# Kernel tuning notes

Measured on AMD Instinct MI355X. Metric: run time of the kernel, lower is better.

The kernel has to match this reference:

```python
import jax, jax.numpy as jnp
import numpy as np


def setup_inputs() -> dict:
    key = jax.random.key(0)
    ks = jax.random.split(key, 5)
    B, H, W, C, R = 4, 64, 64, 256, 32
    x = jax.random.normal(ks[0], (B, H, W, C), dtype=jnp.float32)
    # 1x1 conv kernels stored as [C_in, C_out] matrices (equivalent math)
    w_f = jax.random.normal(ks[1], (C, R), dtype=jnp.float32) * (1.0 / np.sqrt(C))
    w_g = jax.random.normal(ks[2], (C, R), dtype=jnp.float32) * (1.0 / np.sqrt(C))
    w_h = jax.random.normal(ks[3], (C, R), dtype=jnp.float32) * (1.0 / np.sqrt(C))
    w_v = jax.random.normal(ks[4], (R, C), dtype=jnp.float32) * (1.0 / np.sqrt(R))
    gamma = jnp.zeros((1,), dtype=jnp.float32)
    return {"x": x, "w_f": w_f, "w_g": w_g, "w_h": w_h, "w_v": w_v, "gamma": gamma}


def reference(x, w_f, w_g, w_h, w_v, gamma):
    B, H, W, C = x.shape
    N = H * W
    xt = x.reshape(B, N, C)                       # flatten spatial tokens
    f = jnp.einsum('bnc,cr->bnr', xt, w_f)        # 1x1 conv == token-wise matmul
    g = jnp.einsum('bnc,cr->bnr', xt, w_g)
    h = jnp.einsum('bnc,cr->bnr', xt, w_h)
    scores = jnp.einsum('bnr,bmr->bnm', f, g)     # [B, N, N]
    # NOTE: original softmaxes over axis=1 (the query/row axis), not axis=-1
    attn = jax.nn.softmax(scores, axis=1)
    y = jnp.einsum('bnm,bmr->bnr', attn, h)       # [B, N, R]
    y = jnp.einsum('bnr,rc->bnc', y, w_v)         # output 1x1 conv
    y = y.reshape(B, H, W, C)
    return gamma * y + x
```

## Files before the change

kernel.cpp:

```cpp
#include <hip/hip_runtime.h>


#define BB 4
#define NN 4096
#define CC 256
#define RR 32
#define CSEG 4
#define LOG2E 1.44269504088896340736f

typedef short short8 __attribute__((ext_vector_type(8)));
typedef short short4v __attribute__((ext_vector_type(4)));
typedef unsigned short ushort8 __attribute__((ext_vector_type(8)));
typedef float floatx4 __attribute__((ext_vector_type(4)));

#define MFMA16 __builtin_amdgcn_mfma_f32_16x16x32_bf16
#define MFMA16K __builtin_amdgcn_mfma_f32_16x16x16bf16_1k

static __device__ __forceinline__ unsigned short f2bf(float f) {
  union { float f; unsigned u; } v; v.f = f;
  const unsigned r = v.u + 0x7fffu + ((v.u >> 16) & 1u);
  return (unsigned short)(r >> 16);
}
static __device__ __forceinline__ unsigned bfpack(float lo, float hi) {
  return __builtin_amdgcn_perm(__float_as_uint(hi), __float_as_uint(lo), 0x07060302u);
}

__global__ __launch_bounds__(256) void k_prep(
    const float* __restrict__ wf, const float* __restrict__ wg,
    const float* __restrict__ wh, const float* __restrict__ wv,
    unsigned short* __restrict__ wfrag, unsigned short* __restrict__ wvfrag) {
  const int idx = blockIdx.x * 256 + threadIdx.x;
  const int lane = (idx >> 3) & 63;
  const int j = idx & 7;
  const int col = lane & 15, q = lane >> 4;
  if (idx < 24576) {
    const int mat = idx >> 13;
    const int fid = (idx >> 9) & 15;
    const int kc = fid >> 1, nt = fid & 1;
    const float* w = (mat == 0) ? wf : ((mat == 1) ? wg : wh);
    wfrag[idx] = f2bf(w[(kc * 32 + q * 8 + j) * RR + nt * 16 + col]);
  } else {
    const int r = idx - 24576;
    const int t = (r >> 9) & 15;
    wvfrag[r] = f2bf(wv[(q * 8 + j) * CC + t * 16 + col]);
  }
}

__global__ __launch_bounds__(256) void k_fgh(
    const float* __restrict__ x, const unsigned short* __restrict__ wfrag,
    unsigned short* __restrict__ f16, unsigned short* __restrict__ g16,
    unsigned short* __restrict__ hT16) {
  __shared__ unsigned short wflds[24576];
  const int tid = threadIdx.x, lane = tid & 63, wave = tid >> 6;
  const int col = lane & 15, q = lane >> 4;
  {
    const uint4* src = (const uint4*)wfrag;
    uint4* dst = (uint4*)wflds;
#pragma unroll
    for (int i = 0; i < 12; ++i) dst[tid + i * 256] = src[tid + i * 256];
  }
  __syncthreads();
  const int t0 = blockIdx.x * 64 + wave * 16;
  short8 af[8];
  const float* xr = x + (long)(t0 + col) * CC + q * 8;
#pragma unroll
  for (int kc = 0; kc < 8; ++kc) {
    float tmp[8];
    *(float4*)(tmp) = *(const float4*)(xr + kc * 32);
    *(float4*)(tmp + 4) = *(const float4*)(xr + kc * 32 + 4);
    short8 o;
#pragma unroll
    for (int j = 0; j < 8; ++j) o[j] = (short)f2bf(tmp[j]);
    af[kc] = o;
  }
  const floatx4 zero = {0.f, 0.f, 0.f, 0.f};
  floatx4 acc[3][2];
#pragma unroll
  for (int m = 0; m < 3; ++m) { acc[m][0] = zero; acc[m][1] = zero; }
#pragma unroll
  for (int kc = 0; kc < 8; ++kc) {
#pragma unroll
    for (int mat = 0; mat < 3; ++mat) {
#pragma unroll
      for (int nt = 0; nt < 2; ++nt) {
        const short8 bf = *(const short8*)(wflds + (mat * 16 + kc * 2 + nt) * 512 + lane * 8);
        acc[mat][nt] = MFMA16(af[kc], bf, acc[mat][nt], 0, 0, 0);
      }
    }
  }
  const int b = t0 >> 12;
#pragma unroll
  for (int nt = 0; nt < 2; ++nt) {
#pragma unroll
    for (int r = 0; r < 4; ++r) {
      const int tok = t0 + q * 4 + r;
      const int n = nt * 16 + col;
      f16[(long)tok * RR + n] = f2bf(acc[0][nt][r] * LOG2E);
      g16[(long)tok * RR + n] = f2bf(acc[1][nt][r]);
      const int tl = tok & (NN - 1);
      const int sp = (tl & ~31) | (q << 3) | ((tl & 16) >> 2) | r;
      hT16[((long)b * RR + n) * NN + sp] = f2bf(acc[2][nt][r]);
    }
  }
}

__global__ __launch_bounds__(256) void k_colsum(
    const unsigned short* __restrict__ f16, const unsigned short* __restrict__ g16,
    float* __restrict__ psum) {
  const int tid = threadIdx.x, lane = tid & 63, wave = tid >> 6;
  const int col = lane & 15, q = lane >> 4;
  const int mblk = blockIdx.x & 31;
  const int b = (blockIdx.x >> 5) & 3;
  const int seg = blockIdx.x >> 7;
  const int m0 = mblk * 128 + wave * 32;
  const short8 bg1 = *(const short8*)(g16 + ((long)(b * NN + m0 + col)) * RR + q * 8);
  const short8 bg2 = *(const short8*)(g16 + ((long)(b * NN + m0 + 16 + col)) * RR + q * 8);
  const floatx4 zero = {0.f, 0.f, 0.f, 0.f};
  float s1 = 0.f, s2 = 0.f;
  const unsigned short* fb = f16 + ((long)b * NN + seg * (NN / CSEG)) * RR;
#pragma unroll 4
  for (int n = 0; n < NN / CSEG; n += 16) {
    const short8 af = *(const short8*)(fb + (long)(n + col) * RR + q * 8);
    const floatx4 d1 = MFMA16(af, bg1, zero, 0, 0, 0);
    const floatx4 d2 = MFMA16(af, bg2, zero, 0, 0, 0);
    s1 += __builtin_amdgcn_exp2f(d1[0]) + __builtin_amdgcn_exp2f(d1[1]) +
          __builtin_amdgcn_exp2f(d1[2]) + __builtin_amdgcn_exp2f(d1[3]);
    s2 += __builtin_amdgcn_exp2f(d2[0]) + __builtin_amdgcn_exp2f(d2[1]) +
          __builtin_amdgcn_exp2f(d2[2]) + __builtin_amdgcn_exp2f(d2[3]);
  }
  s1 += __shfl_xor(s1, 16); s1 += __shfl_xor(s1, 32);
  s2 += __shfl_xor(s2, 16); s2 += __shfl_xor(s2, 32);
  if (lane < 16) {
    psum[(long)seg * (BB * NN) + b * NN + m0 + lane] = s1;
    psum[(long)seg * (BB * NN) + b * NN + m0 + 16 + lane] = s2;
  }
}

__global__ __launch_bounds__(256) void k_scaleh(
    const float* __restrict__ psum, unsigned short* __restrict__ hT16) {
  const long i8 = ((long)blockIdx.x * 256 + threadIdx.x) * 8;
  const int b = (int)(i8 >> 17);
  const int m = (int)(i8 & (NN - 1));
  const int lo = (m & ~31) | ((m & 24) >> 1);
  float cs[8] = {0.f, 0.f, 0.f, 0.f, 0.f, 0.f, 0.f, 0.f};
#pragma unroll
  for (int sg = 0; sg < CSEG; ++sg) {
    const float* p = psum + (long)sg * (BB * NN) + b * NN;
    const float4 a = *(const float4*)(p + lo);
    const float4 c = *(const float4*)(p + lo + 16);
    cs[0] += a.x; cs[1] += a.y; cs[2] += a.z; cs[3] += a.w;
    cs[4] += c.x; cs[5] += c.y; cs[6] += c.z; cs[7] += c.w;
  }
  const ushort8 hv = *(const ushort8*)(hT16 + i8);
  ushort8 o;
#pragma unroll
  for (int j = 0; j < 8; ++j) {
    const float h = __uint_as_float(((unsigned)hv[j]) << 16);
    o[j] = f2bf(h * __builtin_amdgcn_rcpf(cs[j]));
  }
  *(ushort8*)(hT16 + i8) = o;
}

__global__ __launch_bounds__(512, 4) void k_pvout(
    const unsigned short* __restrict__ f16, const unsigned short* __restrict__ g16,
    const unsigned short* __restrict__ hT16, const unsigned short* __restrict__ wvfrag,
    const float* __restrict__ x, const float* __restrict__ gamma,
    float* __restrict__ out) {
  __shared__ float ylds[8][32 * 36];
  __shared__ float sc_all[8][16 * 36];
  const int tid = threadIdx.x, lane = tid & 63, wave = tid >> 6;
  const int col = lane & 15, q = lane >> 4;
  const int b = blockIdx.x >> 7;
  const int t0 = (blockIdx.x & 127) * 32;
  const floatx4 zero = {0.f, 0.f, 0.f, 0.f};
  const short8 af1 = *(const short8*)(f16 + ((long)(b * NN + t0 + col)) * RR + q * 8);
  const short8 af2 = *(const short8*)(f16 + ((long)(b * NN + t0 + 16 + col)) * RR + q * 8);
  floatx4 a11 = zero, a12 = zero, a21 = zero, a22 = zero;
  const unsigned short* gb = g16 + (long)b * NN * RR;
  const unsigned short* hb = hT16 + (long)b * RR * NN;
  const int mq = wave * 512;
#pragma unroll 2
  for (int mi = 0; mi < 512; mi += 32) {
    const int m0 = mq + mi;
    const short8 bg1 = *(const short8*)(gb + (long)(m0 + col) * RR + q * 8);
    const short8 bg2 = *(const short8*)(gb + (long)(m0 + 16 + col) * RR + q * 8);
    const short8 hv1 = *(const short8*)(hb + (long)col * NN + m0 + q * 8);
    const short8 hv2 = *(const short8*)(hb + (long)(col + 16) * NN + m0 + q * 8);
    const floatx4 d00 = MFMA16(bg1, af1, zero, 0, 0, 0);
    const floatx4 d01 = MFMA16(bg2, af1, zero, 0, 0, 0);
    const floatx4 d10 = MFMA16(bg1, af2, zero, 0, 0, 0);
    const floatx4 d11 = MFMA16(bg2, af2, zero, 0, 0, 0);
    union PU { unsigned u[2]; short4v s; } p00, p01, p10, p11;
    p00.u[0] = bfpack(__builtin_amdgcn_exp2f(d00[0]), __builtin_amdgcn_exp2f(d00[1]));
    p00.u[1] = bfpack(__builtin_amdgcn_exp2f(d00[2]), __builtin_amdgcn_exp2f(d00[3]));
    p01.u[0] = bfpack(__builtin_amdgcn_exp2f(d01[0]), __builtin_amdgcn_exp2f(d01[1]));
    p01.u[1] = bfpack(__builtin_amdgcn_exp2f(d01[2]), __builtin_amdgcn_exp2f(d01[3]));
    p10.u[0] = bfpack(__builtin_amdgcn_exp2f(d10[0]), __builtin_amdgcn_exp2f(d10[1]));
    p10.u[1] = bfpack(__builtin_amdgcn_exp2f(d10[2]), __builtin_amdgcn_exp2f(d10[3]));
    p11.u[0] = bfpack(__builtin_amdgcn_exp2f(d11[0]), __builtin_amdgcn_exp2f(d11[1]));
    p11.u[1] = bfpack(__builtin_amdgcn_exp2f(d11[2]), __builtin_amdgcn_exp2f(d11[3]));
    const short4v bh1lo = __builtin_shufflevector(hv1, hv1, 0, 1, 2, 3);
    const short4v bh1hi = __builtin_shufflevector(hv1, hv1, 4, 5, 6, 7);
    const short4v bh2lo = __builtin_shufflevector(hv2, hv2, 0, 1, 2, 3);
    const short4v bh2hi = __builtin_shufflevector(hv2, hv2, 4, 5, 6, 7);
    a11 = MFMA16K(p00.s, bh1lo, a11, 0, 0, 0);
    a11 = MFMA16K(p01.s, bh1hi, a11, 0, 0, 0);
    a12 = MFMA16K(p00.s, bh2lo, a12, 0, 0, 0);
    a12 = MFMA16K(p01.s, bh2hi, a12, 0, 0, 0);
    a21 = MFMA16K(p10.s, bh1lo, a21, 0, 0, 0);
    a21 = MFMA16K(p11.s, bh1hi, a21, 0, 0, 0);
    a22 = MFMA16K(p10.s, bh2lo, a22, 0, 0, 0);
    a22 = MFMA16K(p11.s, bh2hi, a22, 0, 0, 0);
  }
  {
    float* yp = &ylds[wave][0];
#pragma unroll
    for (int r = 0; r < 4; ++r) {
      yp[(q * 4 + r) * 36 + col] = a11[r];
      yp[(q * 4 + r) * 36 + col + 16] = a12[r];
      yp[(16 + q * 4 + r) * 36 + col] = a21[r];
      yp[(16 + q * 4 + r) * 36 + col + 16] = a22[r];
    }
  }
  __syncthreads();
  {
    const int tile = wave & 1, hh = wave >> 1;
    float s[8] = {0.f, 0.f, 0.f, 0.f, 0.f, 0.f, 0.f, 0.f};
#pragma unroll
    for (int w2 = 0; w2 < 8; ++w2) {
      const float* yp = &ylds[w2][(tile * 16 + col) * 36 + q * 8];
      const float4 u0 = *(const float4*)yp;
      const float4 u1 = *(const float4*)(yp + 4);
      s[0] += u0.x; s[1] += u0.y; s[2] += u0.z; s[3] += u0.w;
      s[4] += u1.x; s[5] += u1.y; s[6] += u1.z; s[7] += u1.w;
    }
    short8 ay;
#pragma unroll
    for (int j = 0; j < 8; ++j) ay[j] = (short)f2bf(s[j]);
    const float gm = gamma[0];
    float* sc = &sc_all[wave][0];
    const int row = lane >> 2, c4 = (lane & 3) * 4;
#pragma unroll
    for (int tp = 0; tp < 4; tp += 2) {
      const short8 bw0 = *(const short8*)(wvfrag + (hh * 4 + tp) * 512 + lane * 8);
      const short8 bw1 = *(const short8*)(wvfrag + (hh * 4 + tp + 1) * 512 + lane * 8);
      const floatx4 d0 = MFMA16(ay, bw0, zero, 0, 0, 0);
      const floatx4 d1 = MFMA16(ay, bw1, zero, 0, 0, 0);
#pragma unroll
      for (int r = 0; r < 4; ++r) {
        sc[(q * 4 + r) * 36 + col] = d0[r];
        sc[(q * 4 + r) * 36 + col + 16] = d1[r];
      }
#pragma unroll
      for (int j = 0; j < 2; ++j) {
        const float4 v = *(const float4*)(sc + row * 36 + c4 + j * 16);
        const long gidx = (long)(b * NN + t0 + tile * 16 + row) * CC +
                          hh * 64 + tp * 16 + j * 16 + c4;
        const float4 xv = *(const float4*)(x + gidx);
        float4 o;
        o.x = gm * v.x + xv.x; o.y = gm * v.y + xv.y;
        o.z = gm * v.z + xv.z; o.w = gm * v.w + xv.w;
        *(float4*)(out + gidx) = o;
      }
    }
  }
}

extern "C" void kernel_launch(void* const* d_in, const int* in_sizes, int n_in,
                              void* d_out, int out_size, void* d_ws, size_t ws_size,
                              hipStream_t stream) {
  const float* x = (const float*)d_in[0];
  const float* wf = (const float*)d_in[1];
  const float* wg = (const float*)d_in[2];
  const float* wh = (const float*)d_in[3];
  const float* wv = (const float*)d_in[4];
  const float* gamma = (const float*)d_in[5];
  float* out = (float*)d_out;

  unsigned short* f16 = (unsigned short*)d_ws;
  unsigned short* g16 = f16 + (long)BB * NN * RR;
  unsigned short* hT16 = g16 + (long)BB * NN * RR;
  unsigned short* wfrag = hT16 + (long)BB * NN * RR;
  unsigned short* wvfrag = wfrag + 24576;
  float* psum = (float*)(wvfrag + 8192);

  k_prep<<<128, 256, 0, stream>>>(wf, wg, wh, wv, wfrag, wvfrag);
  k_fgh<<<BB * NN / 64, 256, 0, stream>>>(x, wfrag, f16, g16, hT16);
  k_colsum<<<CSEG * BB * 32, 256, 0, stream>>>(f16, g16, psum);
  k_scaleh<<<BB * RR * NN / 2048, 256, 0, stream>>>(psum, hT16);
  k_pvout<<<BB * 128, 512, 0, stream>>>(f16, g16, hT16, wvfrag, x, gamma, out);
}
```

Before: 125.0 us.

## Fold softmax normalization into MFMA accumulator and drop prep and scale kernels

```diff
diff --git a/kernel.cpp b/kernel.cpp
--- a/kernel.cpp
+++ b/kernel.cpp
@@ -5,7 +5,6 @@
 #define NN 4096
 #define CC 256
 #define RR 32
-#define CSEG 4
 #define LOG2E 1.44269504088896340736f
 
 typedef short short8 __attribute__((ext_vector_type(8)));
@@ -25,41 +24,31 @@
   return __builtin_amdgcn_perm(__float_as_uint(hi), __float_as_uint(lo), 0x07060302u);
 }
 
-__global__ __launch_bounds__(256) void k_prep(
-    const float* __restrict__ wf, const float* __restrict__ wg,
-    const float* __restrict__ wh, const float* __restrict__ wv,
-    unsigned short* __restrict__ wfrag, unsigned short* __restrict__ wvfrag) {
-  const int idx = blockIdx.x * 256 + threadIdx.x;
-  const int lane = (idx >> 3) & 63;
-  const int j = idx & 7;
-  const int col = lane & 15, q = lane >> 4;
-  if (idx < 24576) {
-    const int mat = idx >> 13;
-    const int fid = (idx >> 9) & 15;
-    const int kc = fid >> 1, nt = fid & 1;
-    const float* w = (mat == 0) ? wf : ((mat == 1) ? wg : wh);
-    wfrag[idx] = f2bf(w[(kc * 32 + q * 8 + j) * RR + nt * 16 + col]);
-  } else {
-    const int r = idx - 24576;
-    const int t = (r >> 9) & 15;
-    wvfrag[r] = f2bf(wv[(q * 8 + j) * CC + t * 16 + col]);
-  }
-}
-
 __global__ __launch_bounds__(256) void k_fgh(
-    const float* __restrict__ x, const unsigned short* __restrict__ wfrag,
+    const float* __restrict__ x, const float* __restrict__ wf,
+    const float* __restrict__ wg, const float* __restrict__ wh,
     unsigned short* __restrict__ f16, unsigned short* __restrict__ g16,
     unsigned short* __restrict__ hT16) {
   __shared__ unsigned short wflds[24576];
   const int tid = threadIdx.x, lane = tid & 63, wave = tid >> 6;
   const int col = lane & 15, q = lane >> 4;
   {
-    const uint4* src = (const uint4*)wfrag;
-    uint4* dst = (uint4*)wflds;
-#pragma unroll
-    for (int i = 0; i < 12; ++i) dst[tid + i * 256] = src[tid + i * 256];
-  }
-  __syncthreads();
+    const float* mats[3] = {wf, wg, wh};
+#pragma unroll
+    for (int mat = 0; mat < 3; ++mat) {
+      const float* w = mats[mat];
+#pragma unroll 4
+      for (int i = 0; i < 32; ++i) {
+        const int idx = mat * 8192 + i * 256 + tid;
+        const int fid = (idx >> 9) & 15;
+        const int kc = fid >> 1, nt = fid & 1;
+        const int l2 = (idx >> 3) & 63;
+        const int c2 = l2 & 15, q2 = l2 >> 4;
+        const int j = idx & 7;
+        wflds[idx] = f2bf(w[(kc * 32 + q2 * 8 + j) * RR + nt * 16 + c2]);
+      }
+    }
+  }
   const int t0 = blockIdx.x * 64 + wave * 16;
   short8 af[8];
   const float* xr = x + (long)(t0 + col) * CC + q * 8;
@@ -73,6 +62,7 @@
     for (int j = 0; j < 8; ++j) o[j] = (short)f2bf(tmp[j]);
     af[kc] = o;
   }
+  __syncthreads();
   const floatx4 zero = {0.f, 0.f, 0.f, 0.f};
   floatx4 acc[3][2];
 #pragma unroll
@@ -106,20 +96,19 @@
 
 __global__ __launch_bounds__(256) void k_colsum(
     const unsigned short* __restrict__ f16, const unsigned short* __restrict__ g16,
-    float* __restrict__ psum) {
+    float* __restrict__ nlg2cs) {
+  __shared__ float red[4][32];
   const int tid = threadIdx.x, lane = tid & 63, wave = tid >> 6;
   const int col = lane & 15, q = lane >> 4;
-  const int mblk = blockIdx.x & 31;
-  const int b = (blockIdx.x >> 5) & 3;
-  const int seg = blockIdx.x >> 7;
-  const int m0 = mblk * 128 + wave * 32;
+  const int b = blockIdx.x >> 7;
+  const int m0 = (blockIdx.x & 127) * 32;
   const short8 bg1 = *(const short8*)(g16 + ((long)(b * NN + m0 + col)) * RR + q * 8);
   const short8 bg2 = *(const short8*)(g16 + ((long)(b * NN + m0 + 16 + col)) * RR + q * 8);
   const floatx4 zero = {0.f, 0.f, 0.f, 0.f};
   float s1 = 0.f, s2 = 0.f;
-  const unsigned short* fb = f16 + ((long)b * NN + seg * (NN / CSEG)) * RR;
+  const unsigned short* fb = f16 + ((long)b * NN + wave * (NN / 4)) * RR;
 #pragma unroll 4
-  for (int n = 0; n < NN / CSEG; n += 16) {
+  for (int n = 0; n < NN / 4; n += 16) {
     const short8 af = *(const short8*)(fb + (long)(n + col) * RR + q * 8);
     const floatx4 d1 = MFMA16(af, bg1, zero, 0, 0, 0);
     const floatx4 d2 = MFMA16(af, bg2, zero, 0, 0, 0);
@@ -131,53 +120,46 @@
   s1 += __shfl_xor(s1, 16); s1 += __shfl_xor(s1, 32);
   s2 += __shfl_xor(s2, 16); s2 += __shfl_xor(s2, 32);
   if (lane < 16) {
-    psum[(long)seg * (BB * NN) + b * NN + m0 + lane] = s1;
-    psum[(long)seg * (BB * NN) + b * NN + m0 + 16 + lane] = s2;
-  }
-}
-
-__global__ __launch_bounds__(256) void k_scaleh(
-    const float* __restrict__ psum, unsigned short* __restrict__ hT16) {
-  const long i8 = ((long)blockIdx.x * 256 + threadIdx.x) * 8;
-  const int b = (int)(i8 >> 17);
-  const int m = (int)(i8 & (NN - 1));
-  const int lo = (m & ~31) | ((m & 24) >> 1);
-  float cs[8] = {0.f, 0.f, 0.f, 0.f, 0.f, 0.f, 0.f, 0.f};
-#pragma unroll
-  for (int sg = 0; sg < CSEG; ++sg) {
-    const float* p = psum + (long)sg * (BB * NN) + b * NN;
-    const float4 a = *(const float4*)(p + lo);
-    const float4 c = *(const float4*)(p + lo + 16);
-    cs[0] += a.x; cs[1] += a.y; cs[2] += a.z; cs[3] += a.w;
-    cs[4] += c.x; cs[5] += c.y; cs[6] += c.z; cs[7] += c.w;
-  }
-  const ushort8 hv = *(const ushort8*)(hT16 + i8);
-  ushort8 o;
-#pragma unroll
-  for (int j = 0; j < 8; ++j) {
-    const float h = __uint_as_float(((unsigned)hv[j]) << 16);
-    o[j] = f2bf(h * __builtin_amdgcn_rcpf(cs[j]));
-  }
-  *(ushort8*)(hT16 + i8) = o;
+    red[wave][lane] = s1;
+    red[wave][lane + 16] = s2;
+  }
+  __syncthreads();
+  if (tid < 32) {
+    const float cs = red[0][tid] + red[1][tid] + red[2][tid] + red[3][tid];
+    nlg2cs[(long)b * NN + m0 + tid] = -__builtin_amdgcn_logf(cs);
+  }
 }
 
 __global__ __launch_bounds__(512, 4) void k_pvout(
     const unsigned short* __restrict__ f16, const unsigned short* __restrict__ g16,
-    const unsigned short* __restrict__ hT16, const unsigned short* __restrict__ wvfrag,
-    const float* __restrict__ x, const float* __restrict__ gamma,
-    float* __restrict__ out) {
+    const unsigned short* __restrict__ hT16, const float* __restrict__ nlg2cs,
+    const float* __restrict__ wv, const float* __restrict__ x,
+    const float* __restrict__ gamma, float* __restrict__ out) {
   __shared__ float ylds[8][32 * 36];
   __shared__ float sc_all[8][16 * 36];
+  __shared__ unsigned short wvlds[8192];
   const int tid = threadIdx.x, lane = tid & 63, wave = tid >> 6;
   const int col = lane & 15, q = lane >> 4;
   const int b = blockIdx.x >> 7;
   const int t0 = (blockIdx.x & 127) * 32;
   const floatx4 zero = {0.f, 0.f, 0.f, 0.f};
+  {
+#pragma unroll 4
+    for (int i = 0; i < 16; ++i) {
+      const int idx = i * 512 + tid;
+      const int t = idx >> 9;
+      const int l2 = (idx >> 3) & 63;
+      const int c2 = l2 & 15, q2 = l2 >> 4;
+      const int j = idx & 7;
+      wvlds[idx] = f2bf(wv[(q2 * 8 + j) * CC + t * 16 + c2]);
+    }
+  }
   const short8 af1 = *(const short8*)(f16 + ((long)(b * NN + t0 + col)) * RR + q * 8);
   const short8 af2 = *(const short8*)(f16 + ((long)(b * NN + t0 + 16 + col)) * RR + q * 8);
   floatx4 a11 = zero, a12 = zero, a21 = zero, a22 = zero;
   const unsigned short* gb = g16 + (long)b * NN * RR;
   const unsigned short* hb = hT16 + (long)b * RR * NN;
+  const float* csb = nlg2cs + (long)b * NN;
   const int mq = wave * 512;
 #pragma unroll 2
   for (int mi = 0; mi < 512; mi += 32) {
@@ -186,10 +168,12 @@
     const short8 bg2 = *(const short8*)(gb + (long)(m0 + 16 + col) * RR + q * 8);
     const short8 hv1 = *(const short8*)(hb + (long)col * NN + m0 + q * 8);
     const short8 hv2 = *(const short8*)(hb + (long)(col + 16) * NN + m0 + q * 8);
-    const floatx4 d00 = MFMA16(bg1, af1, zero, 0, 0, 0);
-    const floatx4 d01 = MFMA16(bg2, af1, zero, 0, 0, 0);
-    const floatx4 d10 = MFMA16(bg1, af2, zero, 0, 0, 0);
-    const floatx4 d11 = MFMA16(bg2, af2, zero, 0, 0, 0);
+    const floatx4 cm0 = *(const floatx4*)(csb + m0 + q * 4);
+    const floatx4 cm1 = *(const floatx4*)(csb + m0 + 16 + q * 4);
+    const floatx4 d00 = MFMA16(bg1, af1, cm0, 0, 0, 0);
+    const floatx4 d01 = MFMA16(bg2, af1, cm1, 0, 0, 0);
+    const floatx4 d10 = MFMA16(bg1, af2, cm0, 0, 0, 0);
+    const floatx4 d11 = MFMA16(bg2, af2, cm1, 0, 0, 0);
     union PU { unsigned u[2]; short4v s; } p00, p01, p10, p11;
     p00.u[0] = bfpack(__builtin_amdgcn_exp2f(d00[0]), __builtin_amdgcn_exp2f(d00[1]));
     p00.u[1] = bfpack(__builtin_amdgcn_exp2f(d00[2]), __builtin_amdgcn_exp2f(d00[3]));
@@ -242,8 +226,8 @@
     const int row = lane >> 2, c4 = (lane & 3) * 4;
 #pragma unroll
     for (int tp = 0; tp < 4; tp += 2) {
-      const short8 bw0 = *(const short8*)(wvfrag + (hh * 4 + tp) * 512 + lane * 8);
-      const short8 bw1 = *(const short8*)(wvfrag + (hh * 4 + tp + 1) * 512 + lane * 8);
+      const short8 bw0 = *(const short8*)(wvlds + (hh * 4 + tp) * 512 + lane * 8);
+      const short8 bw1 = *(const short8*)(wvlds + (hh * 4 + tp + 1) * 512 + lane * 8);
       const floatx4 d0 = MFMA16(ay, bw0, zero, 0, 0, 0);
       const floatx4 d1 = MFMA16(ay, bw1, zero, 0, 0, 0);
 #pragma unroll
@@ -280,13 +264,9 @@
   unsigned short* f16 = (unsigned short*)d_ws;
   unsigned short* g16 = f16 + (long)BB * NN * RR;
   unsigned short* hT16 = g16 + (long)BB * NN * RR;
-  unsigned short* wfrag = hT16 + (long)BB * NN * RR;
-  unsigned short* wvfrag = wfrag + 24576;
-  float* psum = (float*)(wvfrag + 8192);
-
-  k_prep<<<128, 256, 0, stream>>>(wf, wg, wh, wv, wfrag, wvfrag);
-  k_fgh<<<BB * NN / 64, 256, 0, stream>>>(x, wfrag, f16, g16, hT16);
-  k_colsum<<<CSEG * BB * 32, 256, 0, stream>>>(f16, g16, psum);
-  k_scaleh<<<BB * RR * NN / 2048, 256, 0, stream>>>(psum, hT16);
-  k_pvout<<<BB * 128, 512, 0, stream>>>(f16, g16, hT16, wvfrag, x, gamma, out);
-}
+  float* nlg2cs = (float*)(hT16 + (long)BB * NN * RR);
+
+  k_fgh<<<BB * NN / 64, 256, 0, stream>>>(x, wf, wg, wh, f16, g16, hT16);
+  k_colsum<<<BB * NN / 32, 256, 0, stream>>>(f16, g16, nlg2cs);
+  k_pvout<<<BB * 128, 512, 0, stream>>>(f16, g16, hT16, nlg2cs, wv, x, gamma, out);
+}
```

Measured after the change: 132.1 us. +5.7%, slower.

## Fold column-sum normalization into attention as log bias, drop scale-h kernel

Applied to the files above, without the earlier changes.

```diff
diff --git a/kernel.cpp b/kernel.cpp
--- a/kernel.cpp
+++ b/kernel.cpp
@@ -107,19 +107,21 @@
 __global__ __launch_bounds__(256) void k_colsum(
     const unsigned short* __restrict__ f16, const unsigned short* __restrict__ g16,
     float* __restrict__ psum) {
+  __shared__ float red[4][32];
   const int tid = threadIdx.x, lane = tid & 63, wave = tid >> 6;
   const int col = lane & 15, q = lane >> 4;
-  const int mblk = blockIdx.x & 31;
-  const int b = (blockIdx.x >> 5) & 3;
-  const int seg = blockIdx.x >> 7;
-  const int m0 = mblk * 128 + wave * 32;
+  const int mblk = blockIdx.x & 127;
+  const int b = (blockIdx.x >> 7) & 3;
+  const int seg = blockIdx.x >> 9;
+  const int m0 = mblk * 32;
   const short8 bg1 = *(const short8*)(g16 + ((long)(b * NN + m0 + col)) * RR + q * 8);
   const short8 bg2 = *(const short8*)(g16 + ((long)(b * NN + m0 + 16 + col)) * RR + q * 8);
   const floatx4 zero = {0.f, 0.f, 0.f, 0.f};
   float s1 = 0.f, s2 = 0.f;
-  const unsigned short* fb = f16 + ((long)b * NN + seg * (NN / CSEG)) * RR;
+  const unsigned short* fb =
+      f16 + ((long)b * NN + seg * (NN / CSEG) + wave * (NN / CSEG / 4)) * RR;
 #pragma unroll 4
-  for (int n = 0; n < NN / CSEG; n += 16) {
+  for (int n = 0; n < NN / CSEG / 4; n += 16) {
     const short8 af = *(const short8*)(fb + (long)(n + col) * RR + q * 8);
     const floatx4 d1 = MFMA16(af, bg1, zero, 0, 0, 0);
     const floatx4 d2 = MFMA16(af, bg2, zero, 0, 0, 0);
@@ -131,54 +133,49 @@
   s1 += __shfl_xor(s1, 16); s1 += __shfl_xor(s1, 32);
   s2 += __shfl_xor(s2, 16); s2 += __shfl_xor(s2, 32);
   if (lane < 16) {
-    psum[(long)seg * (BB * NN) + b * NN + m0 + lane] = s1;
-    psum[(long)seg * (BB * NN) + b * NN + m0 + 16 + lane] = s2;
-  }
-}
-
-__global__ __launch_bounds__(256) void k_scaleh(
-    const float* __restrict__ psum, unsigned short* __restrict__ hT16) {
-  const long i8 = ((long)blockIdx.x * 256 + threadIdx.x) * 8;
-  const int b = (int)(i8 >> 17);
-  const int m = (int)(i8 & (NN - 1));
-  const int lo = (m & ~31) | ((m & 24) >> 1);
-  float cs[8] = {0.f, 0.f, 0.f, 0.f, 0.f, 0.f, 0.f, 0.f};
-#pragma unroll
-  for (int sg = 0; sg < CSEG; ++sg) {
-    const float* p = psum + (long)sg * (BB * NN) + b * NN;
-    const float4 a = *(const float4*)(p + lo);
-    const float4 c = *(const float4*)(p + lo + 16);
-    cs[0] += a.x; cs[1] += a.y; cs[2] += a.z; cs[3] += a.w;
-    cs[4] += c.x; cs[5] += c.y; cs[6] += c.z; cs[7] += c.w;
-  }
-  const ushort8 hv = *(const ushort8*)(hT16 + i8);
-  ushort8 o;
-#pragma unroll
-  for (int j = 0; j < 8; ++j) {
-    const float h = __uint_as_float(((unsigned)hv[j]) << 16);
-    o[j] = f2bf(h * __builtin_amdgcn_rcpf(cs[j]));
-  }
-  *(ushort8*)(hT16 + i8) = o;
+    red[wave][lane] = s1;
+    red[wave][lane + 16] = s2;
+  }
+  __syncthreads();
+  if (tid < 32) {
+    psum[(long)seg * (BB * NN) + b * NN + m0 + tid] =
+        red[0][tid] + red[1][tid] + red[2][tid] + red[3][tid];
+  }
 }
 
 __global__ __launch_bounds__(512, 4) void k_pvout(
     const unsigned short* __restrict__ f16, const unsigned short* __restrict__ g16,
-    const unsigned short* __restrict__ hT16, const unsigned short* __restrict__ wvfrag,
-    const float* __restrict__ x, const float* __restrict__ gamma,
-    float* __restrict__ out) {
+    const unsigned short* __restrict__ hT16, const float* __restrict__ psum,
+    const unsigned short* __restrict__ wvfrag, const float* __restrict__ x,
+    const float* __restrict__ gamma, float* __restrict__ out) {
   __shared__ float ylds[8][32 * 36];
   __shared__ float sc_all[8][16 * 36];
+  __shared__ float bias[NN];
   const int tid = threadIdx.x, lane = tid & 63, wave = tid >> 6;
   const int col = lane & 15, q = lane >> 4;
   const int b = blockIdx.x >> 7;
   const int t0 = (blockIdx.x & 127) * 32;
   const floatx4 zero = {0.f, 0.f, 0.f, 0.f};
+  {
+    float cs[8] = {0.f, 0.f, 0.f, 0.f, 0.f, 0.f, 0.f, 0.f};
+#pragma unroll
+    for (int sg = 0; sg < CSEG; ++sg) {
+      const float* p = psum + (long)sg * (BB * NN) + b * NN + tid * 8;
+      const float4 a = *(const float4*)p;
+      const float4 c = *(const float4*)(p + 4);
+      cs[0] += a.x; cs[1] += a.y; cs[2] += a.z; cs[3] += a.w;
+      cs[4] += c.x; cs[5] += c.y; cs[6] += c.z; cs[7] += c.w;
+    }
+#pragma unroll
+    for (int j = 0; j < 8; ++j) bias[tid * 8 + j] = -__builtin_amdgcn_logf(cs[j]);
+  }
   const short8 af1 = *(const short8*)(f16 + ((long)(b * NN + t0 + col)) * RR + q * 8);
   const short8 af2 = *(const short8*)(f16 + ((long)(b * NN + t0 + 16 + col)) * RR + q * 8);
   floatx4 a11 = zero, a12 = zero, a21 = zero, a22 = zero;
   const unsigned short* gb = g16 + (long)b * NN * RR;
   const unsigned short* hb = hT16 + (long)b * RR * NN;
   const int mq = wave * 512;
+  __syncthreads();
 #pragma unroll 2
   for (int mi = 0; mi < 512; mi += 32) {
     const int m0 = mq + mi;
@@ -186,10 +183,12 @@
     const short8 bg2 = *(const short8*)(gb + (long)(m0 + 16 + col) * RR + q * 8);
     const short8 hv1 = *(const short8*)(hb + (long)col * NN + m0 + q * 8);
     const short8 hv2 = *(const short8*)(hb + (long)(col + 16) * NN + m0 + q * 8);
-    const floatx4 d00 = MFMA16(bg1, af1, zero, 0, 0, 0);
-    const floatx4 d01 = MFMA16(bg2, af1, zero, 0, 0, 0);
-    const floatx4 d10 = MFMA16(bg1, af2, zero, 0, 0, 0);
-    const floatx4 d11 = MFMA16(bg2, af2, zero, 0, 0, 0);
+    const floatx4 cm0 = *(const floatx4*)(bias + m0 + q * 4);
+    const floatx4 cm1 = *(const floatx4*)(bias + m0 + 16 + q * 4);
+    const floatx4 d00 = MFMA16(bg1, af1, cm0, 0, 0, 0);
+    const floatx4 d01 = MFMA16(bg2, af1, cm1, 0, 0, 0);
+    const floatx4 d10 = MFMA16(bg1, af2, cm0, 0, 0, 0);
+    const floatx4 d11 = MFMA16(bg2, af2, cm1, 0, 0, 0);
     union PU { unsigned u[2]; short4v s; } p00, p01, p10, p11;
     p00.u[0] = bfpack(__builtin_amdgcn_exp2f(d00[0]), __builtin_amdgcn_exp2f(d00[1]));
     p00.u[1] = bfpack(__builtin_amdgcn_exp2f(d00[2]), __builtin_amdgcn_exp2f(d00[3]));
@@ -286,7 +285,6 @@
 
   k_prep<<<128, 256, 0, stream>>>(wf, wg, wh, wv, wfrag, wvfrag);
   k_fgh<<<BB * NN / 64, 256, 0, stream>>>(x, wfrag, f16, g16, hT16);
-  k_colsum<<<CSEG * BB * 32, 256, 0, stream>>>(f16, g16, psum);
-  k_scaleh<<<BB * RR * NN / 2048, 256, 0, stream>>>(psum, hT16);
-  k_pvout<<<BB * 128, 512, 0, stream>>>(f16, g16, hT16, wvfrag, x, gamma, out);
-}
+  k_colsum<<<CSEG * BB * 128, 256, 0, stream>>>(f16, g16, psum);
+  k_pvout<<<BB * 128, 512, 0, stream>>>(f16, g16, hT16, psum, wvfrag, x, gamma, out);
+}
```

Result: faster. 121.2 us (-3.0%).
